# Optimization experiments

Hardware: AMD Instinct MI355X
Metric: run time of the kernel (lower is better)

The kernel has to match this reference:

```python
import jax, jax.numpy as jnp
import numpy as np

B, S, D = 4, 4096, 2048
DC = D // 4       # complexity head hidden
DFF = 4 * D       # inner FFN hidden
MIN_CAP, MAX_CAP = 0.25, 1.0


def setup_inputs() -> dict:
    key = jax.random.key(0)
    ks = jax.random.split(key, 9)
    return {
        "hidden": jax.random.normal(ks[0], (B, S, D), jnp.float32),
        "router_weight": jax.random.normal(ks[1], (D,), jnp.float32) * 0.02,
        "router_bias": jnp.zeros((1,), jnp.float32),
        "comp_w1": jax.random.normal(ks[2], (D, DC), jnp.float32) * 0.02,
        "comp_b1": jnp.zeros((DC,), jnp.float32),
        "comp_w2": jax.random.normal(ks[3], (DC, 1), jnp.float32) * 0.02,
        "comp_b2": jnp.zeros((1,), jnp.float32),
        "ffn_w1": jax.random.normal(ks[4], (D, DFF), jnp.float32) * 0.02,
        "ffn_b1": jnp.zeros((DFF,), jnp.float32),
        "ffn_w2": jax.random.normal(ks[5], (DFF, D), jnp.float32) * 0.02,
        "ffn_b2": jnp.zeros((D,), jnp.float32),
    }


def reference(hidden, router_weight, router_bias, comp_w1, comp_b1, comp_w2,
              comp_b2, ffn_w1, ffn_b1, ffn_w2, ffn_b2):
    b, s, d = hidden.shape
    # complexity head on mean-pooled tokens -> scalar capacity (torch .item())
    pooled = hidden.mean(axis=1)                                   # [B, D]
    ch = jax.nn.gelu(pooled @ comp_w1 + comp_b1, approximate=False)
    complexity = jax.nn.sigmoid(ch @ comp_w2 + comp_b2)            # [B, 1]
    capacity = float(jnp.mean(MIN_CAP + complexity * (MAX_CAP - MIN_CAP)))
    k = int(capacity * s)
    if k == 0:
        return hidden
    # mod_top_k_routing: scalar router logits, per-sequence top-k tokens
    logits = jnp.einsum('bsd,d->bs', hidden, router_weight) + router_bias[0]
    top_logits, indices = jax.lax.top_k(logits, k)                 # [B, k]
    weights = jax.nn.sigmoid(top_logits)                           # [B, k]
    selected = jnp.take_along_axis(hidden, indices[:, :, None], axis=1)  # [B,k,D]
    # inner block: FFN d -> 4d -> d with GELU
    h = jax.nn.gelu(selected @ ffn_w1 + ffn_b1, approximate=False)
    processed = h @ ffn_w2 + ffn_b2                                # [B, k, D]
    # scatter_add weighted results back onto the residual stream
    weighted = processed * weights[:, :, None]
    b_idx = jnp.arange(b)[:, None]                                 # [B, 1]
    output = hidden.at[b_idx, indices].add(weighted)
    return output
```

## Files before the change

kernel.cpp:

```cpp
#include <hip/hip_runtime.h>
#include <hip/hip_bf16.h>
#include <math.h>

#define B_ 4
#define S_ 4096
#define D_ 2048
#define DC_ 512
#define DFF_ 8192

typedef __attribute__((ext_vector_type(8))) __bf16 bf16x8;
typedef __attribute__((ext_vector_type(4))) float f32x4;

__device__ __forceinline__ float gelu_exact(float x) {
    return 0.5f * x * (1.0f + erff(x * 0.70710678118654752f));
}

__device__ __forceinline__ unsigned short f2bf_bits(float f) {
    __hip_bfloat16 h = __float2bfloat16(f);
    return *reinterpret_cast<unsigned short*>(&h);
}

#define GLD16(gptr, lptr) \
    __builtin_amdgcn_global_load_lds( \
        (__attribute__((address_space(1))) void*)(gptr), \
        (__attribute__((address_space(3))) void*)(lptr), 16, 0, 0)

__global__ void pool_partial_k(const float* __restrict__ hidden, float* __restrict__ pp) {
    int d = blockIdx.x * 256 + threadIdx.x;
    int sc = blockIdx.y;
    int b = blockIdx.z;
    const float* base = hidden + ((size_t)b * S_ + (size_t)sc * 512) * D_ + d;
    float s = 0.f;
    #pragma unroll 4
    for (int i = 0; i < 512; ++i) s += base[(size_t)i * D_];
    pp[((size_t)sc * B_ + b) * D_ + d] = s;
}

__global__ void pool_reduce_k(const float* __restrict__ pp, float* __restrict__ pooled) {
    int tid = blockIdx.x * 256 + threadIdx.x;
    int b = tid >> 11;
    int d = tid & (D_ - 1);
    float s = 0.f;
    for (int sc = 0; sc < 8; ++sc) s += pp[((size_t)sc * B_ + b) * D_ + d];
    pooled[tid] = s * (1.0f / (float)S_);
}

__global__ __launch_bounds__(256) void logits_k(const float* __restrict__ hidden,
                                                const float* __restrict__ rw,
                                                const float* __restrict__ rb,
                                                float* __restrict__ logits) {
    int tok = blockIdx.x * 4 + (threadIdx.x >> 6);
    int lane = threadIdx.x & 63;
    const float4* row = (const float4*)(hidden + (size_t)tok * D_);
    const float4* w4 = (const float4*)rw;
    float s = 0.f;
    #pragma unroll
    for (int i = 0; i < 8; ++i) {
        float4 v = row[i * 64 + lane];
        float4 w = w4[i * 64 + lane];
        s += (v.x * w.x + v.y * w.y) + (v.z * w.z + v.w * w.w);
    }
    #pragma unroll
    for (int off = 32; off > 0; off >>= 1) s += __shfl_down(s, off, 64);
    if (lane == 0) logits[tok] = s + rb[0];
}

__global__ void head1_k(const float* __restrict__ pooled, const float* __restrict__ w1,
                        const float* __restrict__ b1, float* __restrict__ ch) {
    int j = blockIdx.x * 256 + threadIdx.x;
    int b = j >> 9, c = j & (DC_ - 1);
    float acc = 0.f;
    for (int i = 0; i < D_; ++i) acc += pooled[b * D_ + i] * w1[(size_t)i * DC_ + c];
    ch[j] = gelu_exact(acc + b1[c]);
}

__global__ void head2_k(const float* __restrict__ ch, const float* __restrict__ w2,
                        const float* __restrict__ b2, int* __restrict__ kbuf) {
    __shared__ float red[4];
    int t = threadIdx.x;
    int b = t >> 6, lane = t & 63;
    float acc = 0.f;
    #pragma unroll
    for (int i = 0; i < 8; ++i) acc += ch[b * DC_ + i * 64 + lane] * w2[i * 64 + lane];
    #pragma unroll
    for (int off = 32; off > 0; off >>= 1) acc += __shfl_down(acc, off, 64);
    if (lane == 0) {
        float z = acc + b2[0];
        float cx = 1.f / (1.f + expf(-z));
        red[b] = 0.25f + cx * 0.75f;
    }
    __syncthreads();
    if (t == 0) {
        float cap = ((red[0] + red[1]) + (red[2] + red[3])) * 0.25f;
        int kk = (int)((double)cap * (double)S_);
        if (kk < 0) kk = 0;
        if (kk > S_) kk = S_;
        kbuf[0] = kk;
    }
}

__global__ __launch_bounds__(256) void select_k(const float* __restrict__ logits,
                                                const int* __restrict__ kbuf,
                                                int* __restrict__ gidx,
                                                float* __restrict__ gwt) {
    int b = blockIdx.x;
    int t = threadIdx.x;
    int k = kbuf[0];
    __shared__ float slog[S_];
    __shared__ unsigned su[S_];
    __shared__ int hist[256];
    __shared__ unsigned sprefix;
    __shared__ int srem;
    __shared__ int sg[256], se[256];

    for (int i = t; i < S_; i += 256) {
        float f = logits[b * S_ + i];
        slog[i] = f;
        unsigned ub = __float_as_uint(f);
        su[i] = (ub & 0x80000000u) ? ~ub : (ub | 0x80000000u);
    }
    if (t == 0) { sprefix = 0u; srem = k; }
    __syncthreads();

    for (int round = 0; round < 4; ++round) {
        int shift = 24 - round * 8;
        hist[t] = 0;
        __syncthreads();
        unsigned pref = sprefix;
        unsigned pmask = (round == 0) ? 0u : ~((1u << (shift + 8)) - 1u);
        for (int i = t; i < S_; i += 256) {
            unsigned u = su[i];
            if ((u & pmask) == (pref & pmask))
                atomicAdd(&hist[(u >> shift) & 255], 1);
        }
        __syncthreads();
        if (t == 0) {
            int rem = srem, run = 0;
            for (int v = 255; v >= 0; --v) {
                int h = hist[v];
                if (run + h >= rem) {
                    srem = rem - run;
                    sprefix = pref | ((unsigned)v << shift);
                    break;
                }
                run += h;
            }
        }
        __syncthreads();
    }
    unsigned T = sprefix;
    int need_eq = srem;

    int base = t * 16;
    int local_gt = 0, local_eq = 0;
    #pragma unroll
    for (int i = 0; i < 16; ++i) {
        unsigned u = su[base + i];
        local_gt += (u > T);
        local_eq += (u == T);
    }
    sg[t] = local_gt; se[t] = local_eq;
    __syncthreads();
    for (int o = 1; o < 256; o <<= 1) {
        int vg = (t >= o) ? sg[t - o] : 0;
        int ve = (t >= o) ? se[t - o] : 0;
        __syncthreads();
        sg[t] += vg; se[t] += ve;
        __syncthreads();
    }
    int gt_excl = sg[t] - local_gt;
    int eq_excl = se[t] - local_eq;
    int total_gt = sg[255];

    int gpos = gt_excl, epos = eq_excl;
    for (int i = 0; i < 16; ++i) {
        int s = base + i;
        unsigned u = su[s];
        int pos = -1;
        if (u > T) pos = gpos++;
        else if (u == T) { if (epos < need_eq) pos = total_gt + epos; epos++; }
        if (pos >= 0) {
            gidx[b * k + pos] = b * S_ + s;
            gwt[b * k + pos] = 1.f / (1.f + expf(-slog[s]));
        }
    }
}

__global__ void gather_k(const float* __restrict__ hidden, const int* __restrict__ gidx,
                         const int* __restrict__ kbuf, __hip_bfloat16* __restrict__ Ag) {
    int tid = blockIdx.x * 256 + threadIdx.x;
    int m = tid >> 9, c4 = tid & 511;
    int M = B_ * kbuf[0];
    if (m >= M) return;
    int row = gidx[m];
    float4 v = ((const float4*)(hidden + (size_t)row * D_))[c4];
    ushort4 o;
    o.x = f2bf_bits(v.x); o.y = f2bf_bits(v.y); o.z = f2bf_bits(v.z); o.w = f2bf_bits(v.w);
    ((ushort4*)Ag)[tid] = o;
}

__global__ void transpose_cvt_k(const float* __restrict__ in, __hip_bfloat16* __restrict__ out,
                                int R, int C) {
    __shared__ float tile[32][33];
    int r0 = blockIdx.y * 32, c0 = blockIdx.x * 32;
    int tx = threadIdx.x, ty = threadIdx.y;
    #pragma unroll
    for (int i = 0; i < 32; i += 8)
        tile[ty + i][tx] = in[(size_t)(r0 + ty + i) * C + (c0 + tx)];
    __syncthreads();
    #pragma unroll
    for (int i = 0; i < 32; i += 8)
        out[(size_t)(c0 + ty + i) * R + (r0 + tx)] = __float2bfloat16(tile[tx][ty + i]);
}

__global__ __launch_bounds__(256) void gemm1_k(const __hip_bfloat16* __restrict__ A,
                                               const __hip_bfloat16* __restrict__ BT,
                                               const float* __restrict__ bias,
                                               __hip_bfloat16* __restrict__ H,
                                               const int* __restrict__ kbuf,
                                               int cBase, int CH) {
    int M = B_ * kbuf[0];
    int m0 = blockIdx.y * 128;
    if (m0 >= M) return;
    int nt = blockIdx.x;
    int n0g = cBase + nt * 128;
    __shared__ __align__(16) __hip_bfloat16 As[128 * 32];
    __shared__ __align__(16) __hip_bfloat16 Bs[128 * 32];
    int t = threadIdx.x;
    int lane = t & 63, wave = t >> 6;
    int wm = (wave & 1) * 64, wn = (wave >> 1) * 64;
    f32x4 acc[4][4] = {};

    int ar0 = t >> 2,            ac0 = (t & 3) * 8;
    int ar1 = (256 + t) >> 2,    ac1 = ((256 + t) & 3) * 8;
    int am0 = m0 + ar0; if (am0 >= M) am0 = M - 1;
    int am1 = m0 + ar1; if (am1 >= M) am1 = M - 1;
    const __hip_bfloat16* aP0 = A + (size_t)am0 * D_ + ac0;
    const __hip_bfloat16* aP1 = A + (size_t)am1 * D_ + ac1;
    const __hip_bfloat16* bP0 = BT + (size_t)(n0g + ar0) * D_ + ac0;
    const __hip_bfloat16* bP1 = BT + (size_t)(n0g + ar1) * D_ + ac1;
    unsigned ldsOff0 = (unsigned)(wave * 64) * 16u;
    unsigned ldsOff1 = 4096u + (unsigned)(wave * 64) * 16u;

    for (int kk = 0; kk < D_; kk += 32) {
        GLD16(aP0 + kk, (char*)As + ldsOff0);
        GLD16(aP1 + kk, (char*)As + ldsOff1);
        GLD16(bP0 + kk, (char*)Bs + ldsOff0);
        GLD16(bP1 + kk, (char*)Bs + ldsOff1);
        __syncthreads();
        bf16x8 af[4], bfr[4];
        #pragma unroll
        for (int i = 0; i < 4; ++i)
            af[i] = *(const bf16x8*)(As + (wm + i * 16 + (lane & 15)) * 32 + (lane >> 4) * 8);
        #pragma unroll
        for (int j = 0; j < 4; ++j)
            bfr[j] = *(const bf16x8*)(Bs + (wn + j * 16 + (lane & 15)) * 32 + (lane >> 4) * 8);
        #pragma unroll
        for (int i = 0; i < 4; ++i)
            #pragma unroll
            for (int j = 0; j < 4; ++j)
                acc[i][j] = __builtin_amdgcn_mfma_f32_16x16x32_bf16(af[i], bfr[j], acc[i][j], 0, 0, 0);
        __syncthreads();
    }

    int qrow = (lane >> 4) * 4, qcol = lane & 15;
    #pragma unroll
    for (int i = 0; i < 4; ++i) {
        #pragma unroll
        for (int j = 0; j < 4; ++j) {
            int cc = wn + j * 16 + qcol;
            float bv = bias[n0g + cc];
            #pragma unroll
            for (int r = 0; r < 4; ++r) {
                int mm = m0 + wm + i * 16 + qrow + r;
                if (mm < M) {
                    float v = acc[i][j][r] + bv;
                    H[(size_t)mm * CH + (nt * 128 + cc)] = __float2bfloat16(gelu_exact(v));
                }
            }
        }
    }
}

__global__ __launch_bounds__(256) void gemm2_k(const __hip_bfloat16* __restrict__ A,
                                               const __hip_bfloat16* __restrict__ BT,
                                               const float* __restrict__ bias,
                                               const int* __restrict__ gidx,
                                               const float* __restrict__ gwt,
                                               float* __restrict__ out,
                                               const int* __restrict__ kbuf,
                                               int cBase, int CH, int first) {
    int M = B_ * kbuf[0];
    int m0 = blockIdx.y * 128;
    if (m0 >= M) return;
    int nt = blockIdx.x;
    int n0 = nt * 128;
    __shared__ __align__(16) __hip_bfloat16 As[128 * 32];
    __shared__ __align__(16) __hip_bfloat16 Bs[128 * 32];
    int t = threadIdx.x;
    int lane = t & 63, wave = t >> 6;
    int wm = (wave & 1) * 64, wn = (wave >> 1) * 64;
    f32x4 acc[4][4] = {};

    int ar0 = t >> 2,            ac0 = (t & 3) * 8;
    int ar1 = (256 + t) >> 2,    ac1 = ((256 + t) & 3) * 8;
    int am0 = m0 + ar0; if (am0 >= M) am0 = M - 1;
    int am1 = m0 + ar1; if (am1 >= M) am1 = M - 1;
    const __hip_bfloat16* aP0 = A + (size_t)am0 * CH + ac0;
    const __hip_bfloat16* aP1 = A + (size_t)am1 * CH + ac1;
    const __hip_bfloat16* bP0 = BT + (size_t)(n0 + ar0) * DFF_ + cBase + ac0;
    const __hip_bfloat16* bP1 = BT + (size_t)(n0 + ar1) * DFF_ + cBase + ac1;
    unsigned ldsOff0 = (unsigned)(wave * 64) * 16u;
    unsigned ldsOff1 = 4096u + (unsigned)(wave * 64) * 16u;

    for (int kk = 0; kk < CH; kk += 32) {
        GLD16(aP0 + kk, (char*)As + ldsOff0);
        GLD16(aP1 + kk, (char*)As + ldsOff1);
        GLD16(bP0 + kk, (char*)Bs + ldsOff0);
        GLD16(bP1 + kk, (char*)Bs + ldsOff1);
        __syncthreads();
        bf16x8 af[4], bfr[4];
        #pragma unroll
        for (int i = 0; i < 4; ++i)
            af[i] = *(const bf16x8*)(As + (wm + i * 16 + (lane & 15)) * 32 + (lane >> 4) * 8);
        #pragma unroll
        for (int j = 0; j < 4; ++j)
            bfr[j] = *(const bf16x8*)(Bs + (wn + j * 16 + (lane & 15)) * 32 + (lane >> 4) * 8);
        #pragma unroll
        for (int i = 0; i < 4; ++i)
            #pragma unroll
            for (int j = 0; j < 4; ++j)
                acc[i][j] = __builtin_amdgcn_mfma_f32_16x16x32_bf16(af[i], bfr[j], acc[i][j], 0, 0, 0);
        __syncthreads();
    }

    int qrow = (lane >> 4) * 4, qcol = lane & 15;
    #pragma unroll
    for (int i = 0; i < 4; ++i) {
        #pragma unroll
        for (int j = 0; j < 4; ++j) {
            int cc = wn + j * 16 + qcol;
            int nglob = n0 + cc;
            float bv = bias[nglob];
            #pragma unroll
            for (int r = 0; r < 4; ++r) {
                int mm = m0 + wm + i * 16 + qrow + r;
                if (mm < M) {
                    int grow = gidx[mm];
                    float wgt = gwt[mm];
                    float v = acc[i][j][r];
                    if (first) v += bv;
                    out[(size_t)grow * D_ + nglob] += wgt * v;
                }
            }
        }
    }
}

extern "C" void kernel_launch(void* const* d_in, const int* in_sizes, int n_in,
                              void* d_out, int out_size, void* d_ws, size_t ws_size,
                              hipStream_t stream) {
    (void)in_sizes; (void)n_in;
    const float* hidden = (const float*)d_in[0];
    const float* rw  = (const float*)d_in[1];
    const float* rb  = (const float*)d_in[2];
    const float* cw1 = (const float*)d_in[3];
    const float* cb1 = (const float*)d_in[4];
    const float* cw2 = (const float*)d_in[5];
    const float* cb2 = (const float*)d_in[6];
    const float* fw1 = (const float*)d_in[7];
    const float* fb1 = (const float*)d_in[8];
    const float* fw2 = (const float*)d_in[9];
    const float* fb2 = (const float*)d_in[10];

    char* ws = (char*)d_ws;
    size_t off = 0;
    auto alloc = [&](size_t bytes) {
        size_t r = (off + 255) & ~(size_t)255;
        off = r + bytes;
        return r;
    };
    size_t o_logits = alloc((size_t)B_ * S_ * 4);
    size_t o_pp     = alloc((size_t)8 * B_ * D_ * 4);
    size_t o_pooled = alloc((size_t)B_ * D_ * 4);
    size_t o_ch     = alloc((size_t)B_ * DC_ * 4);
    size_t o_k      = alloc(256);
    size_t o_gidx   = alloc((size_t)B_ * S_ * 4);
    size_t o_gwt    = alloc((size_t)B_ * S_ * 4);
    size_t o_w1T    = alloc((size_t)D_ * DFF_ * 2);
    size_t o_w2T    = alloc((size_t)D_ * DFF_ * 2);
    size_t o_Ag     = alloc((size_t)B_ * S_ * D_ * 2);
    size_t base     = (off + 255) & ~(size_t)255;
    int CH = DFF_;
    while (CH > 128 && base + (size_t)B_ * S_ * CH * 2 > ws_size) CH >>= 1;
    size_t o_H = alloc((size_t)B_ * S_ * CH * 2);

    float* logits = (float*)(ws + o_logits);
    float* pp     = (float*)(ws + o_pp);
    float* pooled = (float*)(ws + o_pooled);
    float* ch     = (float*)(ws + o_ch);
    int*   kbuf   = (int*)(ws + o_k);
    int*   gidx   = (int*)(ws + o_gidx);
    float* gwt    = (float*)(ws + o_gwt);
    __hip_bfloat16* w1T = (__hip_bfloat16*)(ws + o_w1T);
    __hip_bfloat16* w2T = (__hip_bfloat16*)(ws + o_w2T);
    __hip_bfloat16* Ag  = (__hip_bfloat16*)(ws + o_Ag);
    __hip_bfloat16* H   = (__hip_bfloat16*)(ws + o_H);
    float* out = (float*)d_out;

    pool_partial_k<<<dim3(D_ / 256, 8, B_), 256, 0, stream>>>(hidden, pp);
    pool_reduce_k<<<dim3(B_ * D_ / 256), 256, 0, stream>>>(pp, pooled);
    logits_k<<<dim3(B_ * S_ / 4), 256, 0, stream>>>(hidden, rw, rb, logits);
    head1_k<<<dim3(B_ * DC_ / 256), 256, 0, stream>>>(pooled, cw1, cb1, ch);
    head2_k<<<dim3(1), 256, 0, stream>>>(ch, cw2, cb2, kbuf);
    select_k<<<dim3(B_), 256, 0, stream>>>(logits, kbuf, gidx, gwt);
    gather_k<<<dim3(B_ * S_ * (D_ / 4) / 256), 256, 0, stream>>>(hidden, gidx, kbuf, Ag);
    transpose_cvt_k<<<dim3(DFF_ / 32, D_ / 32), dim3(32, 8), 0, stream>>>(fw1, w1T, D_, DFF_);
    transpose_cvt_k<<<dim3(D_ / 32, DFF_ / 32), dim3(32, 8), 0, stream>>>(fw2, w2T, DFF_, D_);
    hipMemcpyAsync(d_out, (const void*)hidden, (size_t)out_size * 4,
                   hipMemcpyDeviceToDevice, stream);

    int nch = DFF_ / CH;
    for (int c = 0; c < nch; ++c) {
        gemm1_k<<<dim3(CH / 128, B_ * S_ / 128), 256, 0, stream>>>(
            Ag, w1T, fb1, H, kbuf, c * CH, CH);
        gemm2_k<<<dim3(D_ / 128, B_ * S_ / 128), 256, 0, stream>>>(
            H, w2T, fb2, gidx, gwt, out, kbuf, c * CH, CH, c == 0);
    }
}
```

Measured before the change: 1.770 ms.

## Replace FFN GEMMs with 8-wave double-buffered swizzled-LDS pipelined kernel

```diff
diff --git a/kernel.cpp b/kernel.cpp
--- a/kernel.cpp
+++ b/kernel.cpp
@@ -213,144 +213,159 @@
         out[(size_t)(c0 + ty + i) * R + (r0 + tx)] = __float2bfloat16(tile[tx][ty + i]);
 }
 
-__global__ __launch_bounds__(256) void gemm1_k(const __hip_bfloat16* __restrict__ A,
-                                               const __hip_bfloat16* __restrict__ BT,
-                                               const float* __restrict__ bias,
-                                               __hip_bfloat16* __restrict__ H,
-                                               const int* __restrict__ kbuf,
-                                               int cBase, int CH) {
-    int M = B_ * kbuf[0];
-    int m0 = blockIdx.y * 128;
+
+#define FENCE_() asm volatile("" ::: "memory")
+#define BARR_()  do { FENCE_(); __builtin_amdgcn_s_barrier(); FENCE_(); } while (0)
+#define VMW_()   do { if constexpr (BN == 256) asm volatile("s_waitcnt vmcnt(6)" ::: "memory"); \
+                      else                     asm volatile("s_waitcnt vmcnt(5)" ::: "memory"); \
+                      __builtin_amdgcn_sched_barrier(0); } while (0)
+
+template <int BN, int EPI>
+__global__ __launch_bounds__(512, 2) void gemm8p(
+    const __hip_bfloat16* __restrict__ A, int lda,
+    const __hip_bfloat16* __restrict__ BT, int ldb,
+    const float* __restrict__ bias,
+    __hip_bfloat16* __restrict__ Hout, int ldh,
+    float* __restrict__ out,
+    const int* __restrict__ gidx, const float* __restrict__ gwt,
+    const int* __restrict__ kbuf, int K, int first)
+{
+    constexpr int NQ = BN / 128;
+    constexpr int NF = 2 * NQ;
+    constexpr int BUFB = BN * 128;
+    extern __shared__ char lds[];
+
+    const int M = B_ * kbuf[0];
+    const int m0 = blockIdx.y * 256;
     if (m0 >= M) return;
-    int nt = blockIdx.x;
-    int n0g = cBase + nt * 128;
-    __shared__ __align__(16) __hip_bfloat16 As[128 * 32];
-    __shared__ __align__(16) __hip_bfloat16 Bs[128 * 32];
-    int t = threadIdx.x;
-    int lane = t & 63, wave = t >> 6;
-    int wm = (wave & 1) * 64, wn = (wave >> 1) * 64;
-    f32x4 acc[4][4] = {};
-
-    int ar0 = t >> 2,            ac0 = (t & 3) * 8;
-    int ar1 = (256 + t) >> 2,    ac1 = ((256 + t) & 3) * 8;
-    int am0 = m0 + ar0; if (am0 >= M) am0 = M - 1;
-    int am1 = m0 + ar1; if (am1 >= M) am1 = M - 1;
-    const __hip_bfloat16* aP0 = A + (size_t)am0 * D_ + ac0;
-    const __hip_bfloat16* aP1 = A + (size_t)am1 * D_ + ac1;
-    const __hip_bfloat16* bP0 = BT + (size_t)(n0g + ar0) * D_ + ac0;
-    const __hip_bfloat16* bP1 = BT + (size_t)(n0g + ar1) * D_ + ac1;
-    unsigned ldsOff0 = (unsigned)(wave * 64) * 16u;
-    unsigned ldsOff1 = 4096u + (unsigned)(wave * 64) * 16u;
-
-    for (int kk = 0; kk < D_; kk += 32) {
-        GLD16(aP0 + kk, (char*)As + ldsOff0);
-        GLD16(aP1 + kk, (char*)As + ldsOff1);
-        GLD16(bP0 + kk, (char*)Bs + ldsOff0);
-        GLD16(bP1 + kk, (char*)Bs + ldsOff1);
-        __syncthreads();
-        bf16x8 af[4], bfr[4];
+    const int n0 = blockIdx.x * BN;
+
+    const int t = threadIdx.x;
+    const int lane = t & 63;
+    const int wave = t >> 6;
+    const int wr = wave >> 2, wc = wave & 3;
+
+    const int rl = t >> 3;
+    const int cbs = ((t & 7) << 4) ^ ((rl & 7) << 4);
+    const int wchunk = (t >> 6) << 10;
+
+    bf16x8 aR[4][2], bR[NQ][2];
+    f32x4 acc[8][NF] = {};
+
+    auto STG = [&](const __hip_bfloat16* src, int row0, int rowMax, int kcol,
+                   int ld, int ldsoff) {
+        int gr = row0 + rl;
+        if (gr > rowMax) gr = rowMax;
+        GLD16(src + (size_t)gr * ld + (kcol + (cbs >> 1)), lds + ldsoff + wchunk);
+    };
+    auto SA = [&](int buf, int h, int kt) {
+        int bo = buf * 32768 + h * 16384;
+        STG(A, m0 + h * 128,      M - 1, kt * 64, lda, bo);
+        STG(A, m0 + h * 128 + 64, M - 1, kt * 64, lda, bo + 8192);
+    };
+    auto SB = [&](int buf, int v, int kt) {
+        int bo = 65536 + buf * BUFB + v * (BUFB / 2);
+        if constexpr (BN == 256) {
+            STG(BT, n0 + v * 128,      0x7fffffff, kt * 64, ldb, bo);
+            STG(BT, n0 + v * 128 + 64, 0x7fffffff, kt * 64, ldb, bo + 8192);
+        } else {
+            STG(BT, n0 + v * 64, 0x7fffffff, kt * 64, ldb, bo);
+        }
+    };
+    auto RA = [&](int buf, int h) {
+        int bo = buf * 32768;
         #pragma unroll
-        for (int i = 0; i < 4; ++i)
-            af[i] = *(const bf16x8*)(As + (wm + i * 16 + (lane & 15)) * 32 + (lane >> 4) * 8);
+        for (int q = 0; q < 4; ++q) {
+            int row = h * 128 + wr * 64 + q * 16 + (lane & 15);
+            int ro = bo + row * 128;
+            int sw = (row & 7) << 4;
+            #pragma unroll
+            for (int ks = 0; ks < 2; ++ks)
+                aR[q][ks] = *(const bf16x8*)(lds + ro + ((ks * 64 + ((lane >> 4) << 4)) ^ sw));
+        }
+    };
+    auto RB = [&](int buf, int v) {
+        int bo = 65536 + buf * BUFB;
         #pragma unroll
-        for (int j = 0; j < 4; ++j)
-            bfr[j] = *(const bf16x8*)(Bs + (wn + j * 16 + (lane & 15)) * 32 + (lane >> 4) * 8);
+        for (int q = 0; q < NQ; ++q) {
+            int row = v * (BN / 2) + wc * (BN / 8) + q * 16 + (lane & 15);
+            int ro = bo + row * 128;
+            int sw = (row & 7) << 4;
+            #pragma unroll
+            for (int ks = 0; ks < 2; ++ks)
+                bR[q][ks] = *(const bf16x8*)(lds + ro + ((ks * 64 + ((lane >> 4) << 4)) ^ sw));
+        }
+    };
+    auto MM = [&](int h, int v) {
+        __builtin_amdgcn_s_setprio(1);
         #pragma unroll
-        for (int i = 0; i < 4; ++i)
+        for (int mi = 0; mi < 4; ++mi)
             #pragma unroll
-            for (int j = 0; j < 4; ++j)
-                acc[i][j] = __builtin_amdgcn_mfma_f32_16x16x32_bf16(af[i], bfr[j], acc[i][j], 0, 0, 0);
-        __syncthreads();
-    }
-
-    int qrow = (lane >> 4) * 4, qcol = lane & 15;
-    #pragma unroll
-    for (int i = 0; i < 4; ++i) {
-        #pragma unroll
-        for (int j = 0; j < 4; ++j) {
-            int cc = wn + j * 16 + qcol;
-            float bv = bias[n0g + cc];
+            for (int nj = 0; nj < NQ; ++nj)
+                #pragma unroll
+                for (int ks = 0; ks < 2; ++ks)
+                    acc[h * 4 + mi][v * NQ + nj] = __builtin_amdgcn_mfma_f32_16x16x32_bf16(
+                        aR[mi][ks], bR[nj][ks], acc[h * 4 + mi][v * NQ + nj], 0, 0, 0);
+        __builtin_amdgcn_s_setprio(0);
+    };
+
+    const int nkt = K >> 6;
+    const int nit = K >> 7;
+
+    SA(0, 0, 0); SA(0, 1, 0); SB(0, 0, 0); SB(0, 1, 0);
+    SA(1, 0, 1); SB(1, 1, 1); SA(1, 1, 1);
+    VMW_(); BARR_();
+
+    for (int it = 0; it < nit; ++it) {
+        int k1 = 2 * it + 1;
+        int k2 = 2 * it + 2; if (k2 > nkt - 1) k2 = nkt - 1;
+        int k3 = 2 * it + 3; if (k3 > nkt - 1) k3 = nkt - 1;
+        RA(0, 0); RB(0, 0); SB(1, 0, k1); BARR_(); MM(0, 0); BARR_();
+        RB(0, 1);           SA(0, 0, k2); BARR_(); MM(0, 1); BARR_();
+        RA(0, 1);           SB(0, 1, k2); BARR_(); MM(1, 1); BARR_();
+        RB(0, 0);           SA(0, 1, k2); BARR_(); MM(1, 0); VMW_(); BARR_();
+        RA(1, 0); RB(1, 0); SB(0, 0, k2); BARR_(); MM(0, 0); BARR_();
+        RB(1, 1);           SA(1, 0, k3); BARR_(); MM(0, 1); BARR_();
+        RA(1, 1);           SB(1, 1, k3); BARR_(); MM(1, 1); BARR_();
+        RB(1, 0);           SA(1, 1, k3); BARR_(); MM(1, 0); VMW_(); BARR_();
+    }
+    asm volatile("s_waitcnt vmcnt(0)" ::: "memory");
+
+    const int qrow = (lane >> 4) << 2, qcol = lane & 15;
+    #pragma unroll
+    for (int f = 0; f < 8; ++f) {
+        const int h = f >> 2, mi = f & 3;
+        const int mbase = m0 + h * 128 + wr * 64 + mi * 16 + qrow;
+        if constexpr (EPI == 0) {
+            #pragma unroll
+            for (int g = 0; g < NF; ++g) {
+                const int v = g / NQ, nj = g % NQ;
+                const int col = n0 + v * (BN / 2) + wc * (BN / 8) + nj * 16 + qcol;
+                const float bv = bias[col];
+                #pragma unroll
+                for (int r = 0; r < 4; ++r) {
+                    int m = mbase + r;
+                    if (m < M)
+                        Hout[(size_t)m * ldh + col] =
+                            __float2bfloat16(gelu_exact(acc[f][g][r] + bv));
+                }
+            }
+        } else {
             #pragma unroll
             for (int r = 0; r < 4; ++r) {
-                int mm = m0 + wm + i * 16 + qrow + r;
-                if (mm < M) {
-                    float v = acc[i][j][r] + bv;
-                    H[(size_t)mm * CH + (nt * 128 + cc)] = __float2bfloat16(gelu_exact(v));
-                }
-            }
-        }
-    }
-}
-
-__global__ __launch_bounds__(256) void gemm2_k(const __hip_bfloat16* __restrict__ A,
-                                               const __hip_bfloat16* __restrict__ BT,
-                                               const float* __restrict__ bias,
-                                               const int* __restrict__ gidx,
-                                               const float* __restrict__ gwt,
-                                               float* __restrict__ out,
-                                               const int* __restrict__ kbuf,
-                                               int cBase, int CH, int first) {
-    int M = B_ * kbuf[0];
-    int m0 = blockIdx.y * 128;
-    if (m0 >= M) return;
-    int nt = blockIdx.x;
-    int n0 = nt * 128;
-    __shared__ __align__(16) __hip_bfloat16 As[128 * 32];
-    __shared__ __align__(16) __hip_bfloat16 Bs[128 * 32];
-    int t = threadIdx.x;
-    int lane = t & 63, wave = t >> 6;
-    int wm = (wave & 1) * 64, wn = (wave >> 1) * 64;
-    f32x4 acc[4][4] = {};
-
-    int ar0 = t >> 2,            ac0 = (t & 3) * 8;
-    int ar1 = (256 + t) >> 2,    ac1 = ((256 + t) & 3) * 8;
-    int am0 = m0 + ar0; if (am0 >= M) am0 = M - 1;
-    int am1 = m0 + ar1; if (am1 >= M) am1 = M - 1;
-    const __hip_bfloat16* aP0 = A + (size_t)am0 * CH + ac0;
-    const __hip_bfloat16* aP1 = A + (size_t)am1 * CH + ac1;
-    const __hip_bfloat16* bP0 = BT + (size_t)(n0 + ar0) * DFF_ + cBase + ac0;
-    const __hip_bfloat16* bP1 = BT + (size_t)(n0 + ar1) * DFF_ + cBase + ac1;
-    unsigned ldsOff0 = (unsigned)(wave * 64) * 16u;
-    unsigned ldsOff1 = 4096u + (unsigned)(wave * 64) * 16u;
-
-    for (int kk = 0; kk < CH; kk += 32) {
-        GLD16(aP0 + kk, (char*)As + ldsOff0);
-        GLD16(aP1 + kk, (char*)As + ldsOff1);
-        GLD16(bP0 + kk, (char*)Bs + ldsOff0);
-        GLD16(bP1 + kk, (char*)Bs + ldsOff1);
-        __syncthreads();
-        bf16x8 af[4], bfr[4];
-        #pragma unroll
-        for (int i = 0; i < 4; ++i)
-            af[i] = *(const bf16x8*)(As + (wm + i * 16 + (lane & 15)) * 32 + (lane >> 4) * 8);
-        #pragma unroll
-        for (int j = 0; j < 4; ++j)
-            bfr[j] = *(const bf16x8*)(Bs + (wn + j * 16 + (lane & 15)) * 32 + (lane >> 4) * 8);
-        #pragma unroll
-        for (int i = 0; i < 4; ++i)
-            #pragma unroll
-            for (int j = 0; j < 4; ++j)
-                acc[i][j] = __builtin_amdgcn_mfma_f32_16x16x32_bf16(af[i], bfr[j], acc[i][j], 0, 0, 0);
-        __syncthreads();
-    }
-
-    int qrow = (lane >> 4) * 4, qcol = lane & 15;
-    #pragma unroll
-    for (int i = 0; i < 4; ++i) {
-        #pragma unroll
-        for (int j = 0; j < 4; ++j) {
-            int cc = wn + j * 16 + qcol;
-            int nglob = n0 + cc;
-            float bv = bias[nglob];
-            #pragma unroll
-            for (int r = 0; r < 4; ++r) {
-                int mm = m0 + wm + i * 16 + qrow + r;
-                if (mm < M) {
-                    int grow = gidx[mm];
-                    float wgt = gwt[mm];
-                    float v = acc[i][j][r];
-                    if (first) v += bv;
-                    out[(size_t)grow * D_ + nglob] += wgt * v;
+                int m = mbase + r;
+                if (m < M) {
+                    int grow = gidx[m];
+                    float wgt = gwt[m];
+                    float* orow = out + (size_t)grow * D_;
+                    #pragma unroll
+                    for (int g = 0; g < NF; ++g) {
+                        const int v = g / NQ, nj = g % NQ;
+                        const int col = n0 + v * (BN / 2) + wc * (BN / 8) + nj * 16 + qcol;
+                        float vv = acc[f][g][r];
+                        if (first) vv += bias[col];
+                        orow[col] += wgt * vv;
+                    }
                 }
             }
         }
@@ -392,7 +407,7 @@
     size_t o_Ag     = alloc((size_t)B_ * S_ * D_ * 2);
     size_t base     = (off + 255) & ~(size_t)255;
     int CH = DFF_;
-    while (CH > 128 && base + (size_t)B_ * S_ * CH * 2 > ws_size) CH >>= 1;
+    while (CH > 256 && base + (size_t)B_ * S_ * CH * 2 > ws_size) CH >>= 1;
     size_t o_H = alloc((size_t)B_ * S_ * CH * 2);
 
     float* logits = (float*)(ws + o_logits);
@@ -408,6 +423,13 @@
     __hip_bfloat16* H   = (__hip_bfloat16*)(ws + o_H);
     float* out = (float*)d_out;
 
+    hipError_t e;
+    e = hipFuncSetAttribute((const void*)gemm8p<256, 0>,
+                            hipFuncAttributeMaxDynamicSharedMemorySize, 131072);
+    e = hipFuncSetAttribute((const void*)gemm8p<128, 1>,
+                            hipFuncAttributeMaxDynamicSharedMemorySize, 131072);
+    (void)e;
+
     pool_partial_k<<<dim3(D_ / 256, 8, B_), 256, 0, stream>>>(hidden, pp);
     pool_reduce_k<<<dim3(B_ * D_ / 256), 256, 0, stream>>>(pp, pooled);
     logits_k<<<dim3(B_ * S_ / 4), 256, 0, stream>>>(hidden, rw, rb, logits);
@@ -422,9 +444,11 @@
 
     int nch = DFF_ / CH;
     for (int c = 0; c < nch; ++c) {
-        gemm1_k<<<dim3(CH / 128, B_ * S_ / 128), 256, 0, stream>>>(
-            Ag, w1T, fb1, H, kbuf, c * CH, CH);
-        gemm2_k<<<dim3(D_ / 128, B_ * S_ / 128), 256, 0, stream>>>(
-            H, w2T, fb2, gidx, gwt, out, kbuf, c * CH, CH, c == 0);
-    }
-}
+        gemm8p<256, 0><<<dim3(CH / 256, B_ * S_ / 256), 512, 131072, stream>>>(
+            Ag, D_, w1T + (size_t)c * CH * D_, D_, fb1 + c * CH,
+            H, CH, nullptr, nullptr, nullptr, kbuf, D_, 0);
+        gemm8p<128, 1><<<dim3(D_ / 128, B_ * S_ / 256), 512, 98304, stream>>>(
+            H, CH, w2T + (size_t)c * CH, DFF_, fb2,
+            nullptr, 0, out, gidx, gwt, kbuf, CH, c == 0);
+    }
+}
```

Measured after the change: 1.576 ms. -11.0%, faster.
